# Kernel optimization log

Measured on AMD Instinct MI355X. Metric: run time of the kernel, lower is better.

## Reference

```python
import jax, jax.numpy as jnp
import numpy as np

EMBED_DIM = 1024
NUM_HEADS = 16
HEAD_DIM = EMBED_DIM // NUM_HEADS
B, N = 4, 2048


def setup_inputs() -> dict:
    key = jax.random.key(0)
    ks = jax.random.split(key, 9)
    s = 1.0 / np.sqrt(EMBED_DIM)  # mimic sensible init scale
    return {
        "q": jax.random.normal(ks[0], (B, N, EMBED_DIM), dtype=jnp.float32),
        "Wq": jax.random.normal(ks[1], (EMBED_DIM, EMBED_DIM), dtype=jnp.float32) * s,
        "bq": jnp.zeros((EMBED_DIM,), dtype=jnp.float32),
        "Wk": jax.random.normal(ks[2], (EMBED_DIM, EMBED_DIM), dtype=jnp.float32) * s,
        "bk": jnp.zeros((EMBED_DIM,), dtype=jnp.float32),
        "Wv": jax.random.normal(ks[3], (EMBED_DIM, EMBED_DIM), dtype=jnp.float32) * s,
        "bv": jnp.zeros((EMBED_DIM,), dtype=jnp.float32),
        "Wo": jax.random.normal(ks[4], (EMBED_DIM, EMBED_DIM), dtype=jnp.float32) * s,
        "bo": jnp.zeros((EMBED_DIM,), dtype=jnp.float32),
    }


def _split_heads(x):
    # [B, N, C] -> [B, H, N, Dh]
    b, n, _ = x.shape
    return x.reshape(b, n, NUM_HEADS, HEAD_DIM).transpose(0, 2, 1, 3)


def reference(q, Wq, bq, Wk, bk, Wv, bv, Wo, bo):
    b, n, c = q.shape
    # self-attention: k = v = q input; nn.Linear computes x @ W.T + b
    qh = _split_heads(q @ Wq.T + bq)
    kh = _split_heads(q @ Wk.T + bk)
    vh = _split_heads(q @ Wv.T + bv)
    # [B, H, N, N]
    attn_logits = jnp.einsum("bhqd,bhkd->bhqk", qh, kh) / np.sqrt(HEAD_DIM).astype(np.float32)
    attn_scores = jax.nn.softmax(attn_logits, axis=-1)
    # dropout rate 0.0 / eval mode -> identity
    attn_w = jnp.einsum("bhqk,bhkd->bhqd", attn_scores, vh)
    attn_w = attn_w.transpose(0, 2, 1, 3).reshape(b, n, c)  # [B, N, C]
    output = attn_w @ Wo.T + bo
    return (output, attn_w)
```

## Files before the change

kernel.cpp:

```cpp
#include <hip/hip_runtime.h>

typedef float  f32x4  __attribute__((ext_vector_type(4)));
typedef float  f32x16 __attribute__((ext_vector_type(16)));
typedef __bf16 bf16x2 __attribute__((ext_vector_type(2)));
typedef __bf16 bf16x4 __attribute__((ext_vector_type(4)));
typedef __bf16 bf16x8 __attribute__((ext_vector_type(8)));
typedef unsigned int u32;
typedef u32 u32x4 __attribute__((ext_vector_type(4)));

#define MFMA16(a, b, c) __builtin_amdgcn_mfma_f32_16x16x32_bf16((a), (b), (c), 0, 0, 0)
#define MFMA32(a, b, c) __builtin_amdgcn_mfma_f32_32x32x16_bf16((a), (b), (c), 0, 0, 0)

constexpr int EMB  = 1024;
constexpr int NSEQ = 2048;
constexpr int NB   = 4;
constexpr int NH   = 16;
constexpr int DH   = 64;
constexpr size_t HSTRIDE = (size_t)NSEQ * DH;
constexpr size_t MAT     = (size_t)NB * NSEQ * EMB;
constexpr size_t WSZ     = (size_t)EMB * EMB;
constexpr int    BSEQ    = NB * NSEQ;
constexpr float  QSCALE  = 0.18033688011112042f;

__device__ __forceinline__ __bf16 f2bf(float f) { return (__bf16)f; }

__device__ __forceinline__ u32 pkbf(float a, float b) {
  bf16x2 t = {(__bf16)a, (__bf16)b};
  return __builtin_bit_cast(u32, t);
}

__device__ __forceinline__ int swz(int a) { return a ^ (((a >> 7) & 7) << 4); }

__device__ __forceinline__ void gll16(const void* g, void* l) {
  __builtin_amdgcn_global_load_lds((const __attribute__((address_space(1))) unsigned*)g,
                                   (__attribute__((address_space(3))) unsigned*)l, 16, 0, 0);
}

__global__ __launch_bounds__(256) void cvt_all(const float* __restrict__ x,
                                               const float* __restrict__ w0,
                                               const float* __restrict__ w1,
                                               const float* __restrict__ w2,
                                               const float* __restrict__ w3,
                                               __bf16* __restrict__ Xbf,
                                               __bf16* __restrict__ Wbf) {
  const int xblocks = (int)(MAT / 4 / 256);
  const int wslice  = (int)(WSZ / 4 / 256);
  const float* src;
  __bf16* dst;
  size_t idx;
  if (blockIdx.x < (unsigned)xblocks) {
    src = x; dst = Xbf;
    idx = (size_t)blockIdx.x * 256 + threadIdx.x;
  } else {
    int j = blockIdx.x - xblocks;
    int z = j / wslice, r = j % wslice;
    const float* srcs[4] = {w0, w1, w2, w3};
    src = srcs[z];
    dst = Wbf + (size_t)z * WSZ;
    idx = (size_t)r * 256 + threadIdx.x;
  }
  f32x4 v = *reinterpret_cast<const f32x4*>(src + idx * 4);
  bf16x4 o = {f2bf(v[0]), f2bf(v[1]), f2bf(v[2]), f2bf(v[3])};
  *reinterpret_cast<bf16x4*>(dst + idx * 4) = o;
}

__global__ __launch_bounds__(256) void qkv3(const __bf16* __restrict__ Xbf,
                                            const __bf16* __restrict__ Wbf,
                                            const float* __restrict__ bq,
                                            const float* __restrict__ bk,
                                            const float* __restrict__ bv,
                                            __bf16* __restrict__ Qw,
                                            __bf16* __restrict__ Kw,
                                            __bf16* __restrict__ Vtw) {
  __shared__ __align__(16) __bf16 smem[4][128 * 64];
  const int t = threadIdx.x;
  const int lane = t & 63, w = t >> 6;
  const int wr = w >> 1, wc = w & 1;
  const int l15 = lane & 15, g = lane >> 4;

  int flat = blockIdx.x + 8 * blockIdx.y;
  int logical = (flat & 7) * 64 + (flat >> 3);
  const int m0 = (logical >> 3) * 128, n0 = (logical & 7) * 128;

  const char* Ac  = (const char*)Xbf;
  const char* W0c = (const char*)(Wbf + 0 * WSZ);
  const char* W1c = (const char*)(Wbf + 1 * WSZ);
  const char* W2c = (const char*)(Wbf + 2 * WSZ);

  const int srow = lane >> 3;
  const int scol = ((lane & 7) ^ srow) * 16;

  int offA[4][2], offB[4][2];
#pragma unroll
  for (int i = 0; i < 4; ++i)
#pragma unroll
    for (int ks = 0; ks < 2; ++ks) {
      int ra = wr * 64 + i * 16 + l15;
      int rb = wc * 64 + i * 16 + l15;
      offA[i][ks] = (ra * 128 + ((ks * 64 + g * 16) ^ ((l15 & 7) << 4))) >> 1;
      offB[i][ks] = (rb * 128 + ((ks * 64 + g * 16) ^ ((l15 & 7) << 4))) >> 1;
    }

  f32x4 acc[3][4][4];
#pragma unroll
  for (int m = 0; m < 3; ++m)
#pragma unroll
    for (int i = 0; i < 4; ++i)
#pragma unroll
      for (int j = 0; j < 4; ++j) acc[m][i][j] = f32x4{0.f, 0.f, 0.f, 0.f};

#pragma unroll 1
  for (int k0 = 0; k0 < EMB; k0 += 64) {
#pragma unroll
    for (int p = 0; p < 4; ++p) {
      int c = p * 4 + w;
      size_t rowA = (size_t)(m0 + c * 8 + srow) * (EMB * 2) + k0 * 2 + scol;
      size_t rowB = (size_t)(n0 + c * 8 + srow) * (EMB * 2) + k0 * 2 + scol;
      gll16(Ac  + rowA, &smem[0][c * 512]);
      gll16(W0c + rowB, &smem[1][c * 512]);
      gll16(W1c + rowB, &smem[2][c * 512]);
      gll16(W2c + rowB, &smem[3][c * 512]);
    }
    __syncthreads();
#pragma unroll
    for (int ks = 0; ks < 2; ++ks) {
      bf16x8 af[4];
#pragma unroll
      for (int i = 0; i < 4; ++i)
        af[i] = *reinterpret_cast<const bf16x8*>(&smem[0][offA[i][ks]]);
#pragma unroll
      for (int mat = 0; mat < 3; ++mat) {
        bf16x8 bf[4];
#pragma unroll
        for (int i = 0; i < 4; ++i)
          bf[i] = *reinterpret_cast<const bf16x8*>(&smem[mat + 1][offB[i][ks]]);
#pragma unroll
        for (int mi = 0; mi < 4; ++mi)
#pragma unroll
          for (int ni = 0; ni < 4; ++ni)
            acc[mat][mi][ni] = MFMA16(af[mi], bf[ni], acc[mat][mi][ni]);
      }
    }
    __syncthreads();
  }

#pragma unroll
  for (int mi = 0; mi < 4; ++mi)
#pragma unroll
    for (int ni = 0; ni < 4; ++ni) {
      int cg = n0 + wc * 64 + ni * 16 + l15;
      int hh = cg >> 6, d = cg & (DH - 1);
#pragma unroll
      for (int j = 0; j < 4; ++j) {
        int rg = m0 + wr * 64 + mi * 16 + g * 4 + j;
        int bb = rg >> 11, r = rg & (NSEQ - 1);
        size_t hb = (size_t)(bb * NH + hh);
        size_t idx = (hb * NSEQ + r) * DH + d;
        Qw[idx] = f2bf((acc[0][mi][ni][j] + bq[cg]) * QSCALE);
        Kw[idx] = f2bf(acc[1][mi][ni][j] + bk[cg]);
      }
      float bvc = bv[cg];
      int rg0 = m0 + wr * 64 + mi * 16 + g * 4;
      bf16x4 pv = {f2bf(acc[2][mi][ni][0] + bvc), f2bf(acc[2][mi][ni][1] + bvc),
                   f2bf(acc[2][mi][ni][2] + bvc), f2bf(acc[2][mi][ni][3] + bvc)};
      *reinterpret_cast<bf16x4*>(Vtw + (size_t)cg * BSEQ + rg0) = pv;
    }
}

__device__ __forceinline__ void gemm_loop(__bf16* sA, __bf16* sB,
                                          const __bf16* __restrict__ A,
                                          const __bf16* __restrict__ W,
                                          int m0, int n0, f32x4 (&acc)[4][4]) {
  const int t = threadIdx.x;
  const int lane = t & 63, w = t >> 6;
  const int wr = w >> 1, wc = w & 1;
  const int l15 = lane & 15, g = lane >> 4;
  const char* Ac = (const char*)A;
  const char* Wc = (const char*)W;
  const int srow = lane >> 3;
  const int scol = ((lane & 7) ^ srow) * 16;

  int offA[4][2], offB[4][2];
#pragma unroll
  for (int i = 0; i < 4; ++i)
#pragma unroll
    for (int ks = 0; ks < 2; ++ks) {
      int ra = wr * 64 + i * 16 + l15;
      int rb = wc * 64 + i * 16 + l15;
      offA[i][ks] = (ra * 128 + ((ks * 64 + g * 16) ^ ((l15 & 7) << 4))) >> 1;
      offB[i][ks] = (rb * 128 + ((ks * 64 + g * 16) ^ ((l15 & 7) << 4))) >> 1;
    }

#pragma unroll 1
  for (int k0 = 0; k0 < EMB; k0 += 64) {
#pragma unroll
    for (int p = 0; p < 4; ++p) {
      int c = p * 4 + w;
      gll16(Ac + (size_t)(m0 + c * 8 + srow) * (EMB * 2) + k0 * 2 + scol, sA + c * 512);
      gll16(Wc + (size_t)(n0 + c * 8 + srow) * (EMB * 2) + k0 * 2 + scol, sB + c * 512);
    }
    __syncthreads();
    bf16x8 af[4][2], bfr[4][2];
#pragma unroll
    for (int i = 0; i < 4; ++i)
#pragma unroll
      for (int ks = 0; ks < 2; ++ks) {
        af[i][ks]  = *reinterpret_cast<const bf16x8*>(sA + offA[i][ks]);
        bfr[i][ks] = *reinterpret_cast<const bf16x8*>(sB + offB[i][ks]);
      }
#pragma unroll
    for (int ks = 0; ks < 2; ++ks)
#pragma unroll
      for (int mi = 0; mi < 4; ++mi)
#pragma unroll
        for (int ni = 0; ni < 4; ++ni)
          acc[mi][ni] = MFMA16(af[mi][ks], bfr[ni][ks], acc[mi][ni]);
    __syncthreads();
  }
}

__global__ __launch_bounds__(256) void oproj_bf(const __bf16* __restrict__ Abf,
                                                const __bf16* __restrict__ W,
                                                const float* __restrict__ bias,
                                                float* __restrict__ outp) {
  __shared__ __align__(16) __bf16 smem[2][128 * 64];
  int flat = blockIdx.x + 8 * blockIdx.y;
  int logical = (flat & 7) * 64 + (flat >> 3);
  const int m0 = (logical >> 3) * 128, n0 = (logical & 7) * 128;

  f32x4 acc[4][4];
#pragma unroll
  for (int i = 0; i < 4; ++i)
#pragma unroll
    for (int j = 0; j < 4; ++j) acc[i][j] = f32x4{0.f, 0.f, 0.f, 0.f};

  gemm_loop(smem[0], smem[1], Abf, W, m0, n0, acc);

  const int lane = threadIdx.x & 63, w = threadIdx.x >> 6;
  const int wr = w >> 1, wc = w & 1, l15 = lane & 15, g = lane >> 4;
#pragma unroll
  for (int mi = 0; mi < 4; ++mi)
#pragma unroll
    for (int ni = 0; ni < 4; ++ni)
#pragma unroll
      for (int j = 0; j < 4; ++j) {
        int rg = m0 + wr * 64 + mi * 16 + g * 4 + j;
        int cg = n0 + wc * 64 + ni * 16 + l15;
        outp[(size_t)rg * EMB + cg] = acc[mi][ni][j] + bias[cg];
      }
}

__global__ __launch_bounds__(512) void flash_kernel(const __bf16* __restrict__ Qb,
                                                    const __bf16* __restrict__ Kb,
                                                    const __bf16* __restrict__ Vtb,
                                                    float* __restrict__ attnw,
                                                    __bf16* __restrict__ attnw_bf) {
  __shared__ __align__(16) __bf16 lds[2][16384];
  const int t = threadIdx.x;
  const int lane = t & 63, w = t >> 6;
  const int l31 = lane & 31, hi = lane >> 5;

  int flat = blockIdx.x + 8 * (blockIdx.y + NH * blockIdx.z);
  int logical = (flat & 7) * 64 + (flat >> 3);
  const int qt = logical & 7, h = (logical >> 3) & 15, b = logical >> 7;

  const size_t hoff = ((size_t)(b * NH + h)) * HSTRIDE;
  const __bf16* Qh = Qb + hoff;
  const char* Kc = (const char*)(Kb + hoff);
  const char* Vc = (const char*)(Vtb + (size_t)(h * DH) * BSEQ + (size_t)b * NSEQ);
  const int q0 = qt * 256 + w * 32;

  bf16x8 qf[4];
#pragma unroll
  for (int ds = 0; ds < 4; ++ds)
    qf[ds] = *reinterpret_cast<const bf16x8*>(Qh + (size_t)(q0 + l31) * DH + ds * 16 + hi * 8);

  int koff[2][4], voff[4][2];
#pragma unroll
  for (int kt32 = 0; kt32 < 2; ++kt32)
#pragma unroll
    for (int ds = 0; ds < 4; ++ds)
      koff[kt32][ds] = swz((kt32 * 32 + l31) * 128 + ds * 32 + hi * 16) >> 1;
#pragma unroll
  for (int c = 0; c < 4; ++c)
#pragma unroll
    for (int db = 0; db < 2; ++db)
      voff[c][db] = swz((db * 32 + l31) * 128 + c * 32 + hi * 16) >> 1;

  auto stage = [&](int bf, int kt) {
#pragma unroll
    for (int hh = 0; hh < 2; ++hh) {
      int L = w * 1024 + lane * 16;
      int s = swz(L);
      gll16(Kc + (size_t)(kt + hh * 64) * 128 + s, &lds[bf][hh * 4096 + w * 512]);
      int d = s >> 7, rem = s & 127;
      gll16(Vc + (size_t)d * (BSEQ * 2) + (kt + hh * 64) * 2 + rem,
            &lds[bf][8192 + hh * 4096 + w * 512]);
    }
  };

  f32x16 o0{}, o1{}, osum{};
  bf16x8 vones;
#pragma unroll
  for (int i = 0; i < 8; ++i) vones[i] = (__bf16)1.0f;

  stage(0, 0);
  __syncthreads();

#pragma unroll 1
  for (int it = 0; it < NSEQ / 128; ++it) {
    const int cur = it & 1;
    if (it + 1 < NSEQ / 128) stage(cur ^ 1, (it + 1) * 128);

#pragma unroll
    for (int sub = 0; sub < 2; ++sub) {
      const __bf16* Kl = lds[cur] + sub * 4096;
      const __bf16* Vl = lds[cur] + 8192 + sub * 4096;

      bf16x8 kf[2][4];
#pragma unroll
      for (int kt32 = 0; kt32 < 2; ++kt32)
#pragma unroll
        for (int ds = 0; ds < 4; ++ds)
          kf[kt32][ds] = *reinterpret_cast<const bf16x8*>(Kl + koff[kt32][ds]);

      f32x16 s0{}, s1{};
      __builtin_amdgcn_s_setprio(1);
#pragma unroll
      for (int ds = 0; ds < 4; ++ds) s0 = MFMA32(kf[0][ds], qf[ds], s0);
#pragma unroll
      for (int ds = 0; ds < 4; ++ds) s1 = MFMA32(kf[1][ds], qf[ds], s1);
      __builtin_amdgcn_s_setprio(0);

      bf16x8 vf[4][2];
#pragma unroll
      for (int c = 0; c < 4; ++c)
#pragma unroll
        for (int db = 0; db < 2; ++db)
          vf[c][db] = *reinterpret_cast<const bf16x8*>(Vl + voff[c][db]);

#pragma unroll
      for (int r = 0; r < 16; ++r) s0[r] = __builtin_exp2f(s0[r]);
#pragma unroll
      for (int r = 0; r < 16; ++r) s1[r] = __builtin_exp2f(s1[r]);

      u32 pk0[8], pk1[8];
#pragma unroll
      for (int j = 0; j < 8; ++j) pk0[j] = pkbf(s0[2 * j], s0[2 * j + 1]);
#pragma unroll
      for (int j = 0; j < 8; ++j) pk1[j] = pkbf(s1[2 * j], s1[2 * j + 1]);

      auto pv_step = [&](u32& a0, u32& a1, u32& a2, u32& a3, int c) {
        asm("v_permlane32_swap_b32 %0, %1" : "+v"(a0), "+v"(a2));
        asm("v_permlane32_swap_b32 %0, %1" : "+v"(a1), "+v"(a3));
        u32x4 wv = {a0, a1, a2, a3};
        bf16x8 pa = __builtin_bit_cast(bf16x8, wv);
        o0 = MFMA32(pa, vf[c][0], o0);
        o1 = MFMA32(pa, vf[c][1], o1);
        osum = MFMA32(pa, vones, osum);
      };
      __builtin_amdgcn_s_setprio(1);
      pv_step(pk0[0], pk0[1], pk0[2], pk0[3], 0);
      pv_step(pk0[4], pk0[5], pk0[6], pk0[7], 1);
      pv_step(pk1[0], pk1[1], pk1[2], pk1[3], 2);
      pv_step(pk1[4], pk1[5], pk1[6], pk1[7], 3);
      __builtin_amdgcn_s_setprio(0);
    }

    __syncthreads();
  }

#pragma unroll
  for (int r = 0; r < 16; ++r) {
    int qq = (r & 3) + 8 * (r >> 2) + 4 * hi;
    float invq = 1.0f / osum[r];
    int row = q0 + qq;
    float v0 = o0[r] * invq, v1 = o1[r] * invq;
    float* base = attnw + ((size_t)(b * NSEQ + row)) * EMB + h * DH;
    base[l31]      = v0;
    base[32 + l31] = v1;
    __bf16* bb2 = attnw_bf + ((size_t)(b * NSEQ + row)) * EMB + h * DH;
    bb2[l31]      = f2bf(v0);
    bb2[32 + l31] = f2bf(v1);
  }
}

extern "C" void kernel_launch(void* const* d_in, const int* in_sizes, int n_in,
                              void* d_out, int out_size, void* d_ws, size_t ws_size,
                              hipStream_t stream) {
  const float* q  = (const float*)d_in[0];
  const float* Wq = (const float*)d_in[1];
  const float* bq = (const float*)d_in[2];
  const float* Wk = (const float*)d_in[3];
  const float* bk = (const float*)d_in[4];
  const float* Wv = (const float*)d_in[5];
  const float* bv = (const float*)d_in[6];
  const float* Wo = (const float*)d_in[7];
  const float* bo = (const float*)d_in[8];

  float* outp  = (float*)d_out;
  float* attnw = outp + MAT;

  __bf16* Qw   = (__bf16*)d_ws;
  __bf16* Kw   = Qw + MAT;
  __bf16* Vtw  = Qw + 2 * MAT;
  __bf16* Xbf  = Qw + 3 * MAT;
  __bf16* Wbf  = Qw + 4 * MAT;

  const int xblocks = (int)(MAT / 4 / 256);
  const int wblocks = (int)(4 * WSZ / 4 / 256);
  cvt_all<<<xblocks + wblocks, 256, 0, stream>>>(q, Wq, Wk, Wv, Wo, Xbf, Wbf);

  qkv3<<<dim3(8, 64), 256, 0, stream>>>(Xbf, Wbf, bq, bk, bv, Qw, Kw, Vtw);

  flash_kernel<<<dim3(8, NH, NB), 512, 0, stream>>>(Qw, Kw, Vtw, attnw, Xbf);

  oproj_bf<<<dim3(8, 64), 256, 0, stream>>>(Xbf, Wbf + 3 * WSZ, bo, outp);
}
```

Before: 221.2 us.

## Shrink QKV GEMM tile to 128x64 to cut registers and double grid

```diff
diff --git a/kernel.cpp b/kernel.cpp
--- a/kernel.cpp
+++ b/kernel.cpp
@@ -72,40 +72,45 @@
                                             __bf16* __restrict__ Qw,
                                             __bf16* __restrict__ Kw,
                                             __bf16* __restrict__ Vtw) {
-  __shared__ __align__(16) __bf16 smem[4][128 * 64];
+  __shared__ __align__(16) __bf16 sA[128 * 64];
+  __shared__ __align__(16) __bf16 sW[3][64 * 64];
   const int t = threadIdx.x;
   const int lane = t & 63, w = t >> 6;
-  const int wr = w >> 1, wc = w & 1;
   const int l15 = lane & 15, g = lane >> 4;
 
-  int flat = blockIdx.x + 8 * blockIdx.y;
-  int logical = (flat & 7) * 64 + (flat >> 3);
-  const int m0 = (logical >> 3) * 128, n0 = (logical & 7) * 128;
+  int flat = blockIdx.x + 16 * blockIdx.y;
+  int logical = (flat & 7) * 128 + (flat >> 3);
+  const int m0 = (logical >> 4) * 128, n0 = (logical & 15) * 64;
 
   const char* Ac  = (const char*)Xbf;
-  const char* W0c = (const char*)(Wbf + 0 * WSZ);
-  const char* W1c = (const char*)(Wbf + 1 * WSZ);
-  const char* W2c = (const char*)(Wbf + 2 * WSZ);
+  const char* Wc[3] = {(const char*)(Wbf + 0 * WSZ),
+                       (const char*)(Wbf + 1 * WSZ),
+                       (const char*)(Wbf + 2 * WSZ)};
 
   const int srow = lane >> 3;
   const int scol = ((lane & 7) ^ srow) * 16;
 
-  int offA[4][2], offB[4][2];
+  int offA[2][2], offB[4][2];
+#pragma unroll
+  for (int i = 0; i < 2; ++i)
+#pragma unroll
+    for (int ks = 0; ks < 2; ++ks) {
+      int ra = w * 32 + i * 16 + l15;
+      offA[i][ks] = (ra * 128 + ((ks * 64 + g * 16) ^ ((l15 & 7) << 4))) >> 1;
+    }
 #pragma unroll
   for (int i = 0; i < 4; ++i)
 #pragma unroll
     for (int ks = 0; ks < 2; ++ks) {
-      int ra = wr * 64 + i * 16 + l15;
-      int rb = wc * 64 + i * 16 + l15;
-      offA[i][ks] = (ra * 128 + ((ks * 64 + g * 16) ^ ((l15 & 7) << 4))) >> 1;
+      int rb = i * 16 + l15;
       offB[i][ks] = (rb * 128 + ((ks * 64 + g * 16) ^ ((l15 & 7) << 4))) >> 1;
     }
 
-  f32x4 acc[3][4][4];
+  f32x4 acc[3][2][4];
 #pragma unroll
   for (int m = 0; m < 3; ++m)
 #pragma unroll
-    for (int i = 0; i < 4; ++i)
+    for (int i = 0; i < 2; ++i)
 #pragma unroll
       for (int j = 0; j < 4; ++j) acc[m][i][j] = f32x4{0.f, 0.f, 0.f, 0.f};
 
@@ -114,28 +119,31 @@
 #pragma unroll
     for (int p = 0; p < 4; ++p) {
       int c = p * 4 + w;
-      size_t rowA = (size_t)(m0 + c * 8 + srow) * (EMB * 2) + k0 * 2 + scol;
+      gll16(Ac + (size_t)(m0 + c * 8 + srow) * (EMB * 2) + k0 * 2 + scol, sA + c * 512);
+    }
+#pragma unroll
+    for (int p = 0; p < 2; ++p) {
+      int c = p * 4 + w;
       size_t rowB = (size_t)(n0 + c * 8 + srow) * (EMB * 2) + k0 * 2 + scol;
-      gll16(Ac  + rowA, &smem[0][c * 512]);
-      gll16(W0c + rowB, &smem[1][c * 512]);
-      gll16(W1c + rowB, &smem[2][c * 512]);
-      gll16(W2c + rowB, &smem[3][c * 512]);
+#pragma unroll
+      for (int mat = 0; mat < 3; ++mat)
+        gll16(Wc[mat] + rowB, &sW[mat][c * 512]);
     }
     __syncthreads();
 #pragma unroll
     for (int ks = 0; ks < 2; ++ks) {
-      bf16x8 af[4];
-#pragma unroll
-      for (int i = 0; i < 4; ++i)
-        af[i] = *reinterpret_cast<const bf16x8*>(&smem[0][offA[i][ks]]);
+      bf16x8 af[2];
+#pragma unroll
+      for (int i = 0; i < 2; ++i)
+        af[i] = *reinterpret_cast<const bf16x8*>(&sA[offA[i][ks]]);
 #pragma unroll
       for (int mat = 0; mat < 3; ++mat) {
         bf16x8 bf[4];
 #pragma unroll
         for (int i = 0; i < 4; ++i)
-          bf[i] = *reinterpret_cast<const bf16x8*>(&smem[mat + 1][offB[i][ks]]);
-#pragma unroll
-        for (int mi = 0; mi < 4; ++mi)
+          bf[i] = *reinterpret_cast<const bf16x8*>(&sW[mat][offB[i][ks]]);
+#pragma unroll
+        for (int mi = 0; mi < 2; ++mi)
 #pragma unroll
           for (int ni = 0; ni < 4; ++ni)
             acc[mat][mi][ni] = MFMA16(af[mi], bf[ni], acc[mat][mi][ni]);
@@ -144,15 +152,16 @@
     __syncthreads();
   }
 
-#pragma unroll
-  for (int mi = 0; mi < 4; ++mi)
+  const int hh = n0 >> 6;
+#pragma unroll
+  for (int mi = 0; mi < 2; ++mi)
 #pragma unroll
     for (int ni = 0; ni < 4; ++ni) {
-      int cg = n0 + wc * 64 + ni * 16 + l15;
-      int hh = cg >> 6, d = cg & (DH - 1);
+      int cg = n0 + ni * 16 + l15;
+      int d = cg & (DH - 1);
 #pragma unroll
       for (int j = 0; j < 4; ++j) {
-        int rg = m0 + wr * 64 + mi * 16 + g * 4 + j;
+        int rg = m0 + w * 32 + mi * 16 + g * 4 + j;
         int bb = rg >> 11, r = rg & (NSEQ - 1);
         size_t hb = (size_t)(bb * NH + hh);
         size_t idx = (hb * NSEQ + r) * DH + d;
@@ -160,7 +169,7 @@
         Kw[idx] = f2bf(acc[1][mi][ni][j] + bk[cg]);
       }
       float bvc = bv[cg];
-      int rg0 = m0 + wr * 64 + mi * 16 + g * 4;
+      int rg0 = m0 + w * 32 + mi * 16 + g * 4;
       bf16x4 pv = {f2bf(acc[2][mi][ni][0] + bvc), f2bf(acc[2][mi][ni][1] + bvc),
                    f2bf(acc[2][mi][ni][2] + bvc), f2bf(acc[2][mi][ni][3] + bvc)};
       *reinterpret_cast<bf16x4*>(Vtw + (size_t)cg * BSEQ + rg0) = pv;
@@ -300,6 +309,7 @@
   };
 
   f32x16 o0{}, o1{}, osum{};
+  const f32x16 kZero{};
   bf16x8 vones;
 #pragma unroll
   for (int i = 0; i < 8; ++i) vones[i] = (__bf16)1.0f;
@@ -324,12 +334,14 @@
         for (int ds = 0; ds < 4; ++ds)
           kf[kt32][ds] = *reinterpret_cast<const bf16x8*>(Kl + koff[kt32][ds]);
 
-      f32x16 s0{}, s1{};
+      f32x16 s0, s1;
       __builtin_amdgcn_s_setprio(1);
-#pragma unroll
-      for (int ds = 0; ds < 4; ++ds) s0 = MFMA32(kf[0][ds], qf[ds], s0);
-#pragma unroll
-      for (int ds = 0; ds < 4; ++ds) s1 = MFMA32(kf[1][ds], qf[ds], s1);
+      s0 = MFMA32(kf[0][0], qf[0], kZero);
+      s1 = MFMA32(kf[1][0], qf[0], kZero);
+#pragma unroll
+      for (int ds = 1; ds < 4; ++ds) s0 = MFMA32(kf[0][ds], qf[ds], s0);
+#pragma unroll
+      for (int ds = 1; ds < 4; ++ds) s1 = MFMA32(kf[1][ds], qf[ds], s1);
       __builtin_amdgcn_s_setprio(0);
 
       bf16x8 vf[4][2];
@@ -411,7 +423,7 @@
   const int wblocks = (int)(4 * WSZ / 4 / 256);
   cvt_all<<<xblocks + wblocks, 256, 0, stream>>>(q, Wq, Wk, Wv, Wo, Xbf, Wbf);
 
-  qkv3<<<dim3(8, 64), 256, 0, stream>>>(Xbf, Wbf, bq, bk, bv, Qw, Kw, Vtw);
+  qkv3<<<dim3(16, 64), 256, 0, stream>>>(Xbf, Wbf, bq, bk, bv, Qw, Kw, Vtw);
 
   flash_kernel<<<dim3(8, NH, NB), 512, 0, stream>>>(Qw, Kw, Vtw, attnw, Xbf);
 
```

After: 213.7 us, median of 2. 3.4% less time.
